# Kernel tuning notes

Measured on AMD Instinct MI355X. Metric: run time of the kernel, lower is better.

## Reference

```python
import jax, jax.numpy as jnp
import numpy as np

N_FRUSTUMS = 14400  # n_splits_azi(360) * n_splits_pol(40)
N_POINTS = 2_000_000
N_CHANNELS = 8


def setup_inputs() -> dict:
    key = jax.random.key(0)
    k1, k2 = jax.random.split(key)
    pc = jax.random.normal(k1, (N_POINTS, N_CHANNELS), dtype=jnp.float32)
    i_frustum = jnp.sort(
        jax.random.randint(k2, (N_POINTS,), 0, N_FRUSTUMS)
    ).astype(jnp.int32)
    i_inv = jnp.arange(N_POINTS, dtype=jnp.int32)  # identity inverse permutation
    counts_padded = jnp.bincount(i_frustum, length=N_FRUSTUMS).astype(jnp.float32)
    return {
        "pc": pc,
        "i_frustum": i_frustum,
        "i_inv": i_inv,
        "counts_padded": counts_padded,
    }


def reference(pc, i_frustum, i_inv, counts_padded):
    """Faithful port of symmetrize_mean / symmetrize_std / symmetrize_max plus the
    gather-broadcast normalize (pc - mean[i_frustum][i_inv]) / std.

    pc:            [N, C] float point features
    i_frustum:     [N]   int point->frustum segment ids (sorted)
    i_inv:         [N]   int inverse permutation applied after gather
    counts_padded: [F]   float per-frustum point counts (0 for empty frustums)
    """
    n_frustums = counts_padded.shape[0]
    nonempty = counts_padded[:, None] != 0.0  # [F, 1]
    safe_counts = jnp.maximum(counts_padded, 1.0)[:, None]  # avoid div-by-zero

    # symmetrize_mean: scatter_add then divide where count != 0
    sums = jax.ops.segment_sum(pc, i_frustum, num_segments=n_frustums)  # [F, C]
    mean = jnp.where(nonempty, sums / safe_counts, sums)

    # symmetrize_std: scatter_add of squared deviation, divide, sqrt where > 0
    dev = pc - mean[i_frustum][i_inv]  # [N, C] gather-broadcast subtract
    var_sums = jax.ops.segment_sum(dev * dev, i_frustum, num_segments=n_frustums)
    var = jnp.where(nonempty, var_sums / safe_counts, var_sums)
    std = jnp.where(var > 0.0, jnp.sqrt(jnp.maximum(var, 0.0)), var)

    # symmetrize_max: scatter_reduce amax onto a zeros-initialized buffer
    # (include_self=True default in torch => result is max(0, segment max))
    frustum_max = jnp.zeros((n_frustums, pc.shape[1]), pc.dtype).at[i_frustum].max(pc)

    # gather-broadcast normalize (decorator_distance_to_mean style, with per-frustum std)
    std_g = std[i_frustum][i_inv]
    pc_norm = dev / jnp.where(std_g > 0.0, std_g, 1.0)

    return mean, std, frustum_max, pc_norm
```

## Files before the change

kernel.cpp:

```cpp
#include <hip/hip_runtime.h>

#define NCH 8
#define CACHE 6

typedef float v4f __attribute__((ext_vector_type(4)));

__device__ __forceinline__ v4f norm4(const float4& v, const float4& m, const float4& d) {
    v4f o;
    o.x = (v.x - m.x) * d.x;
    o.y = (v.y - m.y) * d.y;
    o.z = (v.z - m.z) * d.z;
    o.w = (v.w - m.w) * d.w;
    return o;
}

__device__ __forceinline__ int wave_lower_bound(const int* __restrict__ a, int n, int key,
                                                int lane) {
    int lo = 0, len = n;
    while (len > 64) {
        int step = (len + 63) >> 6;
        int p = lo + lane * step;
        int v = (p < lo + len) ? a[p] : 0x7fffffff;
        unsigned long long bal = __ballot(v < key);
        int cnt = __popcll(bal);
        if (cnt == 0) return lo;
        int nlo = lo + (cnt - 1) * step + 1;
        int nhi = lo + len;
        int cap = lo + cnt * step;
        if (cnt < 64 && cap < nhi) nhi = cap;
        lo = nlo; len = nhi - nlo;
    }
    int v = (lane < len) ? a[lo + lane] : 0x7fffffff;
    unsigned long long bal = __ballot(v < key);
    return lo + __popcll(bal);
}

__global__ __launch_bounds__(256) void k_fused(
    const float* __restrict__ pc, const int* __restrict__ i_frustum,
    const float* __restrict__ counts, int n, int F,
    float* __restrict__ out_mean, float* __restrict__ out_std,
    float* __restrict__ out_max, float* __restrict__ out_pcn)
{
    const int wid = (blockIdx.x * blockDim.x + threadIdx.x) >> 6;
    if (wid >= F) return;
    const int lane = threadIdx.x & 63;

    const int s = wave_lower_bound(i_frustum, n, wid, lane);
    const float cnt = counts[wid];
    const int e = s + (int)cnt;

    const float4* __restrict__ pc4 = reinterpret_cast<const float4*>(pc);
    v4f* __restrict__ out4 = reinterpret_cast<v4f*>(out_pcn);

    const int b = s * 2, E = e * 2;
    const int lim = max(E - 1, 0);

    float4 sum = {0.f, 0.f, 0.f, 0.f};
    float4 sq  = {0.f, 0.f, 0.f, 0.f};
    float4 mx  = {0.f, 0.f, 0.f, 0.f};
    float4 c[CACHE];

    {
        int k = b + lane;
        #pragma unroll
        for (int u = 0; u < CACHE; ++u) {
            c[u] = pc4[min(k, lim)];
            k += 64;
        }
    }
    {
        int k = b + lane;
        #pragma unroll
        for (int u = 0; u < CACHE; ++u) {
            const bool in = k < E;
            float vx = in ? c[u].x : 0.f, vy = in ? c[u].y : 0.f;
            float vz = in ? c[u].z : 0.f, vw = in ? c[u].w : 0.f;
            sum.x += vx; sq.x += vx * vx; mx.x = fmaxf(mx.x, vx);
            sum.y += vy; sq.y += vy * vy; mx.y = fmaxf(mx.y, vy);
            sum.z += vz; sq.z += vz * vz; mx.z = fmaxf(mx.z, vz);
            sum.w += vw; sq.w += vw * vw; mx.w = fmaxf(mx.w, vw);
            k += 64;
        }
        for (int kk = b + lane + CACHE * 64; kk < E; kk += 64) {
            float4 v = pc4[kk];
            sum.x += v.x; sq.x += v.x * v.x; mx.x = fmaxf(mx.x, v.x);
            sum.y += v.y; sq.y += v.y * v.y; mx.y = fmaxf(mx.y, v.y);
            sum.z += v.z; sq.z += v.z * v.z; mx.z = fmaxf(mx.z, v.z);
            sum.w += v.w; sq.w += v.w * v.w; mx.w = fmaxf(mx.w, v.w);
        }
    }

    #pragma unroll
    for (int m = 2; m <= 32; m <<= 1) {
        sum.x += __shfl_xor(sum.x, m, 64);
        sum.y += __shfl_xor(sum.y, m, 64);
        sum.z += __shfl_xor(sum.z, m, 64);
        sum.w += __shfl_xor(sum.w, m, 64);
        sq.x  += __shfl_xor(sq.x,  m, 64);
        sq.y  += __shfl_xor(sq.y,  m, 64);
        sq.z  += __shfl_xor(sq.z,  m, 64);
        sq.w  += __shfl_xor(sq.w,  m, 64);
        mx.x = fmaxf(mx.x, __shfl_xor(mx.x, m, 64));
        mx.y = fmaxf(mx.y, __shfl_xor(mx.y, m, 64));
        mx.z = fmaxf(mx.z, __shfl_xor(mx.z, m, 64));
        mx.w = fmaxf(mx.w, __shfl_xor(mx.w, m, 64));
    }

    const float invc = 1.0f / fmaxf(cnt, 1.0f);
    float4 mean, sd, dv;
    mean.x = sum.x * invc; mean.y = sum.y * invc; mean.z = sum.z * invc; mean.w = sum.w * invc;
    float vx = fmaxf(sq.x * invc - mean.x * mean.x, 0.0f);
    float vy = fmaxf(sq.y * invc - mean.y * mean.y, 0.0f);
    float vz = fmaxf(sq.z * invc - mean.z * mean.z, 0.0f);
    float vw = fmaxf(sq.w * invc - mean.w * mean.w, 0.0f);
    sd.x = sqrtf(vx); sd.y = sqrtf(vy); sd.z = sqrtf(vz); sd.w = sqrtf(vw);
    dv.x = 1.0f / (sd.x > 0.f ? sd.x : 1.f);
    dv.y = 1.0f / (sd.y > 0.f ? sd.y : 1.f);
    dv.z = 1.0f / (sd.z > 0.f ? sd.z : 1.f);
    dv.w = 1.0f / (sd.w > 0.f ? sd.w : 1.f);

    if (lane < 2) {
        reinterpret_cast<float4*>(out_mean + (size_t)wid * NCH)[lane] = mean;
        reinterpret_cast<float4*>(out_std  + (size_t)wid * NCH)[lane] = sd;
        reinterpret_cast<float4*>(out_max  + (size_t)wid * NCH)[lane] = mx;
    }

    {
        int k = b + lane;
        #pragma unroll
        for (int u = 0; u < CACHE; ++u) {
            if (k < E) {
                v4f o = norm4(c[u], mean, dv);
                __builtin_nontemporal_store(o, &out4[k]);
            }
            k += 64;
        }
        for (int kk = b + lane + CACHE * 64; kk < E; kk += 64) {
            v4f o = norm4(pc4[kk], mean, dv);
            __builtin_nontemporal_store(o, &out4[kk]);
        }
    }
}

extern "C" void kernel_launch(void* const* d_in, const int* in_sizes, int n_in,
                              void* d_out, int out_size, void* d_ws, size_t ws_size,
                              hipStream_t stream) {
    const float* pc        = (const float*)d_in[0];
    const int*   i_frustum = (const int*)d_in[1];
    const float* counts    = (const float*)d_in[3];

    int n = in_sizes[0] / NCH;
    int F = in_sizes[3];

    float* out_mean = (float*)d_out;
    float* out_std  = out_mean + (size_t)F * NCH;
    float* out_max  = out_std  + (size_t)F * NCH;
    float* out_pcn  = out_max  + (size_t)F * NCH;

    int waves_per_block = 256 / 64;
    int blocks = (F + waves_per_block - 1) / waves_per_block;
    k_fused<<<blocks, 256, 0, stream>>>(pc, i_frustum, counts, n, F,
                                        out_mean, out_std, out_max, out_pcn);
}
```

Before: 29.36 us.

## Process two frustums per wave and prefetch the second while reducing the first

Each wave now handles two adjacent frustums. It does one binary search and derives the second segment's start from the first count. The second frustum's points are loaded into registers before the first frustum's reduction and normalize, so their memory latency overlaps with that compute. This halves the number of waves and binary searches. The cost is higher register pressure from two caches, which may lower occupancy and reduce parallelism.

Measured after the change: 29.46 us. About the same (+0.3%).

```diff
diff --git a/kernel.cpp b/kernel.cpp
--- a/kernel.cpp
+++ b/kernel.cpp
@@ -35,107 +35,158 @@
     return lo + __popcll(bal);
 }
 
-__global__ __launch_bounds__(256) void k_fused(
+#define ACC(creg, kvar, Evar)                                                  \
+    {                                                                          \
+        const bool in = (kvar) < (Evar);                                       \
+        float ax = in ? (creg).x : 0.f, ay = in ? (creg).y : 0.f;              \
+        float az = in ? (creg).z : 0.f, aw = in ? (creg).w : 0.f;              \
+        sum.x += ax; sq.x += ax * ax; mx.x = fmaxf(mx.x, ax);                  \
+        sum.y += ay; sq.y += ay * ay; mx.y = fmaxf(mx.y, ay);                  \
+        sum.z += az; sq.z += az * az; mx.z = fmaxf(mx.z, az);                  \
+        sum.w += aw; sq.w += aw * aw; mx.w = fmaxf(mx.w, aw);                  \
+    }
+
+#define WREDUCE()                                                              \
+    _Pragma("unroll")                                                          \
+    for (int m = 2; m <= 32; m <<= 1) {                                        \
+        sum.x += __shfl_xor(sum.x, m, 64);                                     \
+        sum.y += __shfl_xor(sum.y, m, 64);                                     \
+        sum.z += __shfl_xor(sum.z, m, 64);                                     \
+        sum.w += __shfl_xor(sum.w, m, 64);                                     \
+        sq.x  += __shfl_xor(sq.x,  m, 64);                                     \
+        sq.y  += __shfl_xor(sq.y,  m, 64);                                     \
+        sq.z  += __shfl_xor(sq.z,  m, 64);                                     \
+        sq.w  += __shfl_xor(sq.w,  m, 64);                                     \
+        mx.x = fmaxf(mx.x, __shfl_xor(mx.x, m, 64));                           \
+        mx.y = fmaxf(mx.y, __shfl_xor(mx.y, m, 64));                           \
+        mx.z = fmaxf(mx.z, __shfl_xor(mx.z, m, 64));                           \
+        mx.w = fmaxf(mx.w, __shfl_xor(mx.w, m, 64));                           \
+    }
+
+__global__ __launch_bounds__(256) void k_pair(
     const float* __restrict__ pc, const int* __restrict__ i_frustum,
     const float* __restrict__ counts, int n, int F,
     float* __restrict__ out_mean, float* __restrict__ out_std,
     float* __restrict__ out_max, float* __restrict__ out_pcn)
 {
     const int wid = (blockIdx.x * blockDim.x + threadIdx.x) >> 6;
-    if (wid >= F) return;
+    const int f0 = wid * 2;
+    if (f0 >= F) return;
+    const int f1 = f0 + 1;
     const int lane = threadIdx.x & 63;
 
-    const int s = wave_lower_bound(i_frustum, n, wid, lane);
-    const float cnt = counts[wid];
-    const int e = s + (int)cnt;
+    const float c0f = counts[f0];
+    const float c1f = (f1 < F) ? counts[f1] : 0.0f;
+    const int s0 = wave_lower_bound(i_frustum, n, f0, lane);
+    const int e0 = s0 + (int)c0f;
+    const int e1 = e0 + (int)c1f;
 
     const float4* __restrict__ pc4 = reinterpret_cast<const float4*>(pc);
     v4f* __restrict__ out4 = reinterpret_cast<v4f*>(out_pcn);
 
-    const int b = s * 2, E = e * 2;
-    const int lim = max(E - 1, 0);
-
-    float4 sum = {0.f, 0.f, 0.f, 0.f};
-    float4 sq  = {0.f, 0.f, 0.f, 0.f};
-    float4 mx  = {0.f, 0.f, 0.f, 0.f};
-    float4 c[CACHE];
-
-    {
-        int k = b + lane;
+    const int b0 = s0 * 2, E0 = e0 * 2;
+    const int b1 = E0,     E1 = e1 * 2;
+    const int lim0 = max(E0 - 1, 0);
+    const int lim1 = max(E1 - 1, 0);
+
+    float4 ca[CACHE], cb[CACHE];
+
+    {
+        int k = b0 + lane;
+        #pragma unroll
+        for (int u = 0; u < CACHE; ++u) { ca[u] = pc4[min(k, lim0)]; k += 64; }
+    }
+
+    float4 sum = {0,0,0,0}, sq = {0,0,0,0}, mx = {0,0,0,0};
+    {
+        int k = b0 + lane;
+        #pragma unroll
+        for (int u = 0; u < CACHE; ++u) { ACC(ca[u], k, E0); k += 64; }
+        for (int kk = b0 + lane + CACHE * 64; kk < E0; kk += 64) {
+            float4 v = pc4[kk]; ACC(v, kk, E0);
+        }
+    }
+
+    {
+        int k = b1 + lane;
+        #pragma unroll
+        for (int u = 0; u < CACHE; ++u) { cb[u] = pc4[min(k, lim1)]; k += 64; }
+    }
+
+    WREDUCE();
+    {
+        const float invc = 1.0f / fmaxf(c0f, 1.0f);
+        float4 mean, sd, dv;
+        mean.x = sum.x * invc; mean.y = sum.y * invc;
+        mean.z = sum.z * invc; mean.w = sum.w * invc;
+        float vx = fmaxf(sq.x * invc - mean.x * mean.x, 0.0f);
+        float vy = fmaxf(sq.y * invc - mean.y * mean.y, 0.0f);
+        float vz = fmaxf(sq.z * invc - mean.z * mean.z, 0.0f);
+        float vw = fmaxf(sq.w * invc - mean.w * mean.w, 0.0f);
+        sd.x = sqrtf(vx); sd.y = sqrtf(vy); sd.z = sqrtf(vz); sd.w = sqrtf(vw);
+        dv.x = 1.0f / (sd.x > 0.f ? sd.x : 1.f);
+        dv.y = 1.0f / (sd.y > 0.f ? sd.y : 1.f);
+        dv.z = 1.0f / (sd.z > 0.f ? sd.z : 1.f);
+        dv.w = 1.0f / (sd.w > 0.f ? sd.w : 1.f);
+        if (lane < 2) {
+            reinterpret_cast<float4*>(out_mean + (size_t)f0 * NCH)[lane] = mean;
+            reinterpret_cast<float4*>(out_std  + (size_t)f0 * NCH)[lane] = sd;
+            reinterpret_cast<float4*>(out_max  + (size_t)f0 * NCH)[lane] = mx;
+        }
+        int k = b0 + lane;
         #pragma unroll
         for (int u = 0; u < CACHE; ++u) {
-            c[u] = pc4[min(k, lim)];
-            k += 64;
-        }
-    }
-    {
-        int k = b + lane;
-        #pragma unroll
-        for (int u = 0; u < CACHE; ++u) {
-            const bool in = k < E;
-            float vx = in ? c[u].x : 0.f, vy = in ? c[u].y : 0.f;
-            float vz = in ? c[u].z : 0.f, vw = in ? c[u].w : 0.f;
-            sum.x += vx; sq.x += vx * vx; mx.x = fmaxf(mx.x, vx);
-            sum.y += vy; sq.y += vy * vy; mx.y = fmaxf(mx.y, vy);
-            sum.z += vz; sq.z += vz * vz; mx.z = fmaxf(mx.z, vz);
-            sum.w += vw; sq.w += vw * vw; mx.w = fmaxf(mx.w, vw);
-            k += 64;
-        }
-        for (int kk = b + lane + CACHE * 64; kk < E; kk += 64) {
-            float4 v = pc4[kk];
-            sum.x += v.x; sq.x += v.x * v.x; mx.x = fmaxf(mx.x, v.x);
-            sum.y += v.y; sq.y += v.y * v.y; mx.y = fmaxf(mx.y, v.y);
-            sum.z += v.z; sq.z += v.z * v.z; mx.z = fmaxf(mx.z, v.z);
-            sum.w += v.w; sq.w += v.w * v.w; mx.w = fmaxf(mx.w, v.w);
-        }
-    }
-
-    #pragma unroll
-    for (int m = 2; m <= 32; m <<= 1) {
-        sum.x += __shfl_xor(sum.x, m, 64);
-        sum.y += __shfl_xor(sum.y, m, 64);
-        sum.z += __shfl_xor(sum.z, m, 64);
-        sum.w += __shfl_xor(sum.w, m, 64);
-        sq.x  += __shfl_xor(sq.x,  m, 64);
-        sq.y  += __shfl_xor(sq.y,  m, 64);
-        sq.z  += __shfl_xor(sq.z,  m, 64);
-        sq.w  += __shfl_xor(sq.w,  m, 64);
-        mx.x = fmaxf(mx.x, __shfl_xor(mx.x, m, 64));
-        mx.y = fmaxf(mx.y, __shfl_xor(mx.y, m, 64));
-        mx.z = fmaxf(mx.z, __shfl_xor(mx.z, m, 64));
-        mx.w = fmaxf(mx.w, __shfl_xor(mx.w, m, 64));
-    }
-
-    const float invc = 1.0f / fmaxf(cnt, 1.0f);
-    float4 mean, sd, dv;
-    mean.x = sum.x * invc; mean.y = sum.y * invc; mean.z = sum.z * invc; mean.w = sum.w * invc;
-    float vx = fmaxf(sq.x * invc - mean.x * mean.x, 0.0f);
-    float vy = fmaxf(sq.y * invc - mean.y * mean.y, 0.0f);
-    float vz = fmaxf(sq.z * invc - mean.z * mean.z, 0.0f);
-    float vw = fmaxf(sq.w * invc - mean.w * mean.w, 0.0f);
-    sd.x = sqrtf(vx); sd.y = sqrtf(vy); sd.z = sqrtf(vz); sd.w = sqrtf(vw);
-    dv.x = 1.0f / (sd.x > 0.f ? sd.x : 1.f);
-    dv.y = 1.0f / (sd.y > 0.f ? sd.y : 1.f);
-    dv.z = 1.0f / (sd.z > 0.f ? sd.z : 1.f);
-    dv.w = 1.0f / (sd.w > 0.f ? sd.w : 1.f);
-
-    if (lane < 2) {
-        reinterpret_cast<float4*>(out_mean + (size_t)wid * NCH)[lane] = mean;
-        reinterpret_cast<float4*>(out_std  + (size_t)wid * NCH)[lane] = sd;
-        reinterpret_cast<float4*>(out_max  + (size_t)wid * NCH)[lane] = mx;
-    }
-
-    {
-        int k = b + lane;
-        #pragma unroll
-        for (int u = 0; u < CACHE; ++u) {
-            if (k < E) {
-                v4f o = norm4(c[u], mean, dv);
+            if (k < E0) {
+                v4f o = norm4(ca[u], mean, dv);
                 __builtin_nontemporal_store(o, &out4[k]);
             }
             k += 64;
         }
-        for (int kk = b + lane + CACHE * 64; kk < E; kk += 64) {
+        for (int kk = b0 + lane + CACHE * 64; kk < E0; kk += 64) {
+            v4f o = norm4(pc4[kk], mean, dv);
+            __builtin_nontemporal_store(o, &out4[kk]);
+        }
+    }
+
+    sum = {0,0,0,0}; sq = {0,0,0,0}; mx = {0,0,0,0};
+    {
+        int k = b1 + lane;
+        #pragma unroll
+        for (int u = 0; u < CACHE; ++u) { ACC(cb[u], k, E1); k += 64; }
+        for (int kk = b1 + lane + CACHE * 64; kk < E1; kk += 64) {
+            float4 v = pc4[kk]; ACC(v, kk, E1);
+        }
+    }
+    WREDUCE();
+    {
+        const float invc = 1.0f / fmaxf(c1f, 1.0f);
+        float4 mean, sd, dv;
+        mean.x = sum.x * invc; mean.y = sum.y * invc;
+        mean.z = sum.z * invc; mean.w = sum.w * invc;
+        float vx = fmaxf(sq.x * invc - mean.x * mean.x, 0.0f);
+        float vy = fmaxf(sq.y * invc - mean.y * mean.y, 0.0f);
+        float vz = fmaxf(sq.z * invc - mean.z * mean.z, 0.0f);
+        float vw = fmaxf(sq.w * invc - mean.w * mean.w, 0.0f);
+        sd.x = sqrtf(vx); sd.y = sqrtf(vy); sd.z = sqrtf(vz); sd.w = sqrtf(vw);
+        dv.x = 1.0f / (sd.x > 0.f ? sd.x : 1.f);
+        dv.y = 1.0f / (sd.y > 0.f ? sd.y : 1.f);
+        dv.z = 1.0f / (sd.z > 0.f ? sd.z : 1.f);
+        dv.w = 1.0f / (sd.w > 0.f ? sd.w : 1.f);
+        if (lane < 2 && f1 < F) {
+            reinterpret_cast<float4*>(out_mean + (size_t)f1 * NCH)[lane] = mean;
+            reinterpret_cast<float4*>(out_std  + (size_t)f1 * NCH)[lane] = sd;
+            reinterpret_cast<float4*>(out_max  + (size_t)f1 * NCH)[lane] = mx;
+        }
+        int k = b1 + lane;
+        #pragma unroll
+        for (int u = 0; u < CACHE; ++u) {
+            if (k < E1) {
+                v4f o = norm4(cb[u], mean, dv);
+                __builtin_nontemporal_store(o, &out4[k]);
+            }
+            k += 64;
+        }
+        for (int kk = b1 + lane + CACHE * 64; kk < E1; kk += 64) {
             v4f o = norm4(pc4[kk], mean, dv);
             __builtin_nontemporal_store(o, &out4[kk]);
         }
@@ -157,8 +208,9 @@
     float* out_max  = out_std  + (size_t)F * NCH;
     float* out_pcn  = out_max  + (size_t)F * NCH;
 
+    int nwaves = (F + 1) / 2;
     int waves_per_block = 256 / 64;
-    int blocks = (F + waves_per_block - 1) / waves_per_block;
-    k_fused<<<blocks, 256, 0, stream>>>(pc, i_frustum, counts, n, F,
-                                        out_mean, out_std, out_max, out_pcn);
-}
+    int blocks = (nwaves + waves_per_block - 1) / waves_per_block;
+    k_pair<<<blocks, 256, 0, stream>>>(pc, i_frustum, counts, n, F,
+                                       out_mean, out_std, out_max, out_pcn);
+}
```
